# Performance work log

Hardware: AMD Instinct MI355X
Metric: run time of the kernel (lower is better)

## Reference

```python
import jax, jax.numpy as jnp
import numpy as np

NS, NC, T, NB = 32, 16, 64, 512
NSC = NS + NC


def setup_inputs() -> dict:
    key = jax.random.key(0)
    k1, k2, k3, k4, k5 = jax.random.split(key, 5)
    # SPD cost matrices so Quu is invertible (as assumed by the LQR math)
    L = jax.random.normal(k1, (NB, T, NSC, NSC), jnp.float32) * 0.1
    Q = L @ jnp.swapaxes(L, -1, -2) + jnp.eye(NSC, dtype=jnp.float32)
    p = jax.random.normal(k2, (NB, T, NSC), jnp.float32)
    x_init = jax.random.normal(k3, (NB, NS), jnp.float32)
    # stable-ish LTI dynamics
    A = 0.9 * jnp.eye(NS, dtype=jnp.float32) + 0.01 * jax.random.normal(k4, (NS, NS), jnp.float32)
    B = 0.1 * jax.random.normal(k5, (NS, NC), jnp.float32)
    dt = jnp.float32(0.1)
    return {"x_init": x_init, "Q": Q, "p": p, "A": A, "B": B, "dt": dt}


def _lqr(x_init, Q, p, A, B):
    ns, nc = A.shape[0], B.shape[1]
    nb, Th = Q.shape[0], Q.shape[1]
    dtype = Q.dtype

    # --- nominal rollout with zero control: x_{t+1} = A x_t ---
    def roll(x, _):
        return x @ A.T, x
    _, cx = jax.lax.scan(roll, x_init, None, length=Th)   # [T,B,ns] states x_0..x_{T-1}
    cu = jnp.zeros((Th, nb, nc), dtype)                    # current_u = 0
    xu = jnp.concatenate([cx, cu], -1)                     # [T,B,nsc]

    Qs = jnp.swapaxes(Q, 0, 1)                             # [T,B,nsc,nsc]
    ps = jnp.swapaxes(p, 0, 1)                             # [T,B,nsc]
    p_new = jnp.einsum('tbij,tbj->tbi', Qs, xu) + ps       # [T,B,nsc]

    F = jnp.concatenate([A, B], axis=1)                    # [ns, nsc]

    # --- backward Riccati recursion (V=v=0 at t=T-1 makes Qt=Q[T-1]) ---
    def bwd(carry, inp):
        V, v = carry                                       # [B,ns,ns], [B,ns]
        Qt_in, qt_in = inp
        Qt = Qt_in + jnp.einsum('si,bst,tj->bij', F, V, F)
        qt = qt_in + v @ F                                 # F^T v
        Qxx, Qxu = Qt[:, :ns, :ns], Qt[:, :ns, ns:]
        Qux, Quu = Qt[:, ns:, :ns], Qt[:, ns:, ns:]
        qx, qu = qt[:, :ns], qt[:, ns:]
        Quu_inv = jnp.linalg.pinv(Quu)
        Kt = -Quu_inv @ Qux                                # [B,nc,ns]
        kt = -jnp.einsum('bij,bj->bi', Quu_inv, qu)        # [B,nc]
        KtT = jnp.swapaxes(Kt, -1, -2)
        Vn = Qxx + Qxu @ Kt + KtT @ Qux + KtT @ Quu @ Kt
        vn = (qx + jnp.einsum('bij,bj->bi', Qxu, kt)
              + jnp.einsum('bij,bj->bi', KtT, qu)
              + jnp.einsum('bij,bj->bi', KtT @ Quu, kt))
        return (Vn, vn), (Kt, kt)

    V0 = jnp.zeros((nb, ns, ns), dtype)
    v0 = jnp.zeros((nb, ns), dtype)
    _, (Ks, ks) = jax.lax.scan(bwd, (V0, v0), (Qs, p_new), reverse=True)

    # --- forward rollout with feedback policy ---
    def fwd(carry, inp):
        xt, cost = carry
        Kt, kt, cxt, cut, Qt, pt = inp
        dut = jnp.einsum('bij,bj->bi', Kt, xt - cxt) + kt
        ut = dut + cut
        xut = jnp.concatenate([xt, ut], -1)
        cost = cost + 0.5 * jnp.einsum('bi,bij,bj->b', xut, Qt, xut) + (xut * pt).sum(-1)
        xn = xt @ A.T + ut @ B.T
        return (xn, cost), (xt, ut)

    (_, cost), (xs, us) = jax.lax.scan(
        fwd, (x_init, jnp.zeros(nb, dtype)), (Ks, ks, cx, cu, Qs, ps))
    x = jnp.swapaxes(xs, 0, 1)   # [B,T,ns]  (states x_0..x_{T-1}, matching x[...,:-1,:])
    u = jnp.swapaxes(us, 0, 1)   # [B,T,nc]
    return x, u, cost


def reference(x_init, Q, p, A, B, dt):
    # dt only matters for nonlinear relinearization; with constant LTI (A,B) it is unused.
    return _lqr(x_init, Q, p, A, B)
```

## Files before the change

kernel.cpp:

```cpp
#include <hip/hip_runtime.h>


#define NSd 32
#define NCd 16
#define Td 64
#define NBd 512
#define NSCd 48

typedef __bf16 bf16x8 __attribute__((ext_vector_type(8)));
typedef __bf16 bf16x4 __attribute__((ext_vector_type(4)));
typedef float f32x4 __attribute__((ext_vector_type(4)));

#define MFMA16(a, b, c) __builtin_amdgcn_mfma_f32_16x16x32_bf16(a, b, c, 0, 0, 0)

#define XOFF ((size_t)0)
#define UOFF ((size_t)NBd * Td * NSd)
#define COFF (UOFF + (size_t)NBd * Td * NCd)

__device__ __forceinline__ float rdl(float v, int l) {
  return __uint_as_float(__builtin_amdgcn_readlane(__float_as_uint(v), l));
}

__global__ __launch_bounds__(256, 3) void lqr_kernel(
    const float* __restrict__ x_init, const float* __restrict__ Qg,
    const float* __restrict__ pg, const float* __restrict__ Ag,
    const float* __restrict__ Bg, float* __restrict__ out,
    float* __restrict__ wsK, float* __restrict__ wskv) {
  const int b = blockIdx.x;
  const int tid = threadIdx.x;
  const int w = tid >> 6;
  const int lane = tid & 63;
  const int fn = lane & 15;
  const int quad = lane >> 4;
  const int k0 = quad * 8;

  __shared__ __attribute__((aligned(16))) float sQ[2304];
  __shared__ float scx[Td][NSd];
  __shared__ float sFf[NSd][NSCd];
  __shared__ __attribute__((aligned(16))) __bf16 sFTh[NSCd][32], sFTl[NSCd][32];
  __shared__ __attribute__((aligned(16))) __bf16 sVh[NSd][32], sVl[NSd][32];
  __shared__ __attribute__((aligned(16))) __bf16 sWTh[NSCd][32], sWTl[NSCd][32];
  __shared__ __attribute__((aligned(16))) __bf16 sXh[NSd][32], sXl[NSd][32];
  __shared__ __attribute__((aligned(16))) __bf16 sKTh[NSd][32], sKTl[NSd][32];
  __shared__ float sQuu[16][17];
  __shared__ float sqt[NSCd];
  __shared__ float svv[NSd];
  __shared__ __attribute__((aligned(16))) float sKT2[NSd][NCd];
  __shared__ float skt2[NCd], spf[2][NSCd];
  __shared__ float sxu[NSCd], sred[NSCd], ssx[NSd];

  for (int idx = tid; idx < 1536; idx += 256) {
    int i = idx / 48, j = idx - i * 48;
    sFf[i][j] = (j < 32) ? Ag[i * 32 + j] : Bg[i * 16 + (j - 32)];
  }
  for (int idx = tid; idx < 1536; idx += 256) {
    int a = idx >> 5, k = idx & 31;
    float f = (a < 32) ? Ag[k * 32 + a] : Bg[k * 16 + (a - 32)];
    __bf16 h = (__bf16)f;
    sFTh[a][k] = h;
    sFTl[a][k] = (__bf16)(f - (float)h);
  }
  for (int idx = tid; idx < 1024; idx += 256) {
    int r = idx >> 5, c = idx & 31;
    __bf16 z = (__bf16)0.f;
    sVh[r][c] = z; sVl[r][c] = z;
    sXh[r][c] = z; sXl[r][c] = z;
    sKTh[r][c] = z; sKTl[r][c] = z;
  }
  if (tid < 32) {
    float xi = x_init[b * 32 + tid];
    scx[0][tid] = xi;
    ssx[tid] = xi;
    svv[tid] = 0.f;
  }
  {
    const float4* src = (const float4*)(Qg + ((size_t)b * Td + 63) * 2304);
    float4* dst = (float4*)sQ;
    dst[tid] = src[tid];
    dst[tid + 256] = src[tid + 256];
    if (tid < 64) dst[tid + 512] = src[tid + 512];
  }
  float ppf = 0.f;
  if (w == 3 && lane < 48) ppf = pg[((size_t)b * Td + 63) * 48 + lane];
  __syncthreads();

  if (w == 0) {
    for (int t2 = 0; t2 < Td - 1; ++t2) {
      if (lane < 32) {
        float acc = 0.f;
#pragma unroll
        for (int j = 0; j < 32; j += 4) {
          float4 a4 = *(const float4*)&sFf[lane][j];
          acc += a4.x * scx[t2][j] + a4.y * scx[t2][j + 1] +
                 a4.z * scx[t2][j + 2] + a4.w * scx[t2][j + 3];
        }
        scx[t2 + 1][lane] = acc;
      }
    }
  }
  __syncthreads();

  for (int t = Td - 1; t >= 0; --t) {
    float4 pf0, pf1, pf2;
    float ppfn;
    if (t > 0) {
      const float4* src = (const float4*)(Qg + ((size_t)b * Td + (t - 1)) * 2304);
      pf0 = src[tid];
      pf1 = src[tid + 256];
      if (tid < 64) pf2 = src[tid + 512];
      if (w == 3 && lane < 48) ppfn = pg[((size_t)b * Td + t - 1) * 48 + lane];
    }
    if (w < 3) {
      const int I = w;
      bf16x8 aH = *(const bf16x8*)&sFTh[16 * I + fn][k0];
      bf16x8 aL = *(const bf16x8*)&sFTl[16 * I + fn][k0];
#pragma unroll
      for (int J = 0; J < 2; ++J) {
        bf16x8 bH = *(const bf16x8*)&sVh[16 * J + fn][k0];
        bf16x8 bL = *(const bf16x8*)&sVl[16 * J + fn][k0];
        f32x4 acc = {0.f, 0.f, 0.f, 0.f};
        acc = MFMA16(aL, bH, acc);
        acc = MFMA16(aH, bL, acc);
        acc = MFMA16(aH, bH, acc);
#pragma unroll
        for (int r = 0; r < 4; ++r) {
          float v = acc[r];
          __bf16 h = (__bf16)v;
          sWTh[16 * I + 4 * quad + r][16 * J + fn] = h;
          sWTl[16 * I + 4 * quad + r][16 * J + fn] = (__bf16)(v - (float)h);
        }
      }
    } else if (lane < 48) {
      float acc = ppf;
#pragma unroll
      for (int k = 0; k < 32; ++k) acc += sQ[k * 48 + lane] * scx[t][k];
#pragma unroll
      for (int k = 0; k < 32; ++k) acc += svv[k] * sFf[k][lane];
      sqt[lane] = acc;
    }
    if (t > 0 && w == 3) ppf = ppfn;
    __syncthreads();

    f32x4 accQ = {0.f, 0.f, 0.f, 0.f};
    if (w < 2) {
      const int I = w;
      bf16x8 aH = *(const bf16x8*)&sWTh[16 * I + fn][k0];
      bf16x8 aL = *(const bf16x8*)&sWTl[16 * I + fn][k0];
      {
        bf16x8 bH = *(const bf16x8*)&sFTh[16 * I + fn][k0];
        bf16x8 bL = *(const bf16x8*)&sFTl[16 * I + fn][k0];
#pragma unroll
        for (int r = 0; r < 4; ++r)
          accQ[r] = sQ[(16 * I + 4 * quad + r) * 48 + 16 * I + fn];
        accQ = MFMA16(aL, bH, accQ);
        accQ = MFMA16(aH, bL, accQ);
        accQ = MFMA16(aH, bH, accQ);
      }
      {
        bf16x8 bH = *(const bf16x8*)&sFTh[32 + fn][k0];
        bf16x8 bL = *(const bf16x8*)&sFTl[32 + fn][k0];
        f32x4 acc;
#pragma unroll
        for (int r = 0; r < 4; ++r)
          acc[r] = sQ[(16 * I + 4 * quad + r) * 48 + 32 + fn];
        acc = MFMA16(aL, bH, acc);
        acc = MFMA16(aH, bL, acc);
        acc = MFMA16(aH, bH, acc);
#pragma unroll
        for (int r = 0; r < 4; ++r) {
          float v = acc[r];
          __bf16 h = (__bf16)v;
          sXh[16 * I + 4 * quad + r][fn] = h;
          sXl[16 * I + 4 * quad + r][fn] = (__bf16)(v - (float)h);
        }
      }
    } else if (w == 2) {
      bf16x8 aH = *(const bf16x8*)&sWTh[fn][k0];
      bf16x8 aL = *(const bf16x8*)&sWTl[fn][k0];
      bf16x8 bH = *(const bf16x8*)&sFTh[16 + fn][k0];
      bf16x8 bL = *(const bf16x8*)&sFTl[16 + fn][k0];
#pragma unroll
      for (int r = 0; r < 4; ++r)
        accQ[r] = sQ[(4 * quad + r) * 48 + 16 + fn];
      accQ = MFMA16(aL, bH, accQ);
      accQ = MFMA16(aH, bL, accQ);
      accQ = MFMA16(aH, bH, accQ);
    } else {
      bf16x8 aH = *(const bf16x8*)&sWTh[32 + fn][k0];
      bf16x8 aL = *(const bf16x8*)&sWTl[32 + fn][k0];
      bf16x8 bH = *(const bf16x8*)&sFTh[32 + fn][k0];
      bf16x8 bL = *(const bf16x8*)&sFTl[32 + fn][k0];
      f32x4 acc;
#pragma unroll
      for (int r = 0; r < 4; ++r)
        acc[r] = sQ[(32 + 4 * quad + r) * 48 + 32 + fn];
      acc = MFMA16(aL, bH, acc);
      acc = MFMA16(aH, bL, acc);
      acc = MFMA16(aH, bH, acc);
#pragma unroll
      for (int r = 0; r < 4; ++r) sQuu[4 * quad + r][fn] = acc[r];
    }
    __syncthreads();

    if (t > 0) {
      float4* dst = (float4*)sQ;
      dst[tid] = pf0;
      dst[tid + 256] = pf1;
      if (tid < 64) dst[tid + 512] = pf2;
    }

    float rhs[16];
    if (lane < 32) {
      bf16x8 xh0 = *(const bf16x8*)&sXh[lane][0];
      bf16x8 xh1 = *(const bf16x8*)&sXh[lane][8];
      bf16x8 xl0 = *(const bf16x8*)&sXl[lane][0];
      bf16x8 xl1 = *(const bf16x8*)&sXl[lane][8];
#pragma unroll
      for (int i = 0; i < 8; ++i) {
        rhs[i] = (float)xh0[i] + (float)xl0[i];
        rhs[8 + i] = (float)xh1[i] + (float)xl1[i];
      }
    } else {
#pragma unroll
      for (int i = 0; i < 16; ++i) rhs[i] = sqt[32 + i];
    }
    float quu[16];
#pragma unroll
    for (int i = 0; i < 16; ++i) quu[i] = sQuu[i][fn];
#pragma unroll
    for (int r = 0; r < 15; ++r) {
      float inv = __builtin_amdgcn_rcpf(rdl(quu[r], r));
#pragma unroll
      for (int i = r + 1; i < 16; ++i) {
        float m = rdl(quu[i], r) * inv;
        rhs[i] -= m * rhs[r];
        quu[i] -= m * quu[r];
      }
    }
    float xx[16];
#pragma unroll
    for (int r = 15; r >= 0; --r) {
      float s = rhs[r];
#pragma unroll
      for (int c = r + 1; c < 16; ++c) s -= rdl(quu[r], c) * xx[c];
      xx[r] = s * __builtin_amdgcn_rcpf(rdl(quu[r], r));
    }
    if (lane < 32) {
      bf16x8 h0, l0, h1, l1;
#pragma unroll
      for (int u = 0; u < 8; ++u) {
        float kv = -xx[u];
        __bf16 hh = (__bf16)kv;
        h0[u] = hh; l0[u] = (__bf16)(kv - (float)hh);
        float kv2 = -xx[8 + u];
        __bf16 hh2 = (__bf16)kv2;
        h1[u] = hh2; l1[u] = (__bf16)(kv2 - (float)hh2);
      }
      *(bf16x8*)&sKTh[lane][0] = h0;
      *(bf16x8*)&sKTh[lane][8] = h1;
      *(bf16x8*)&sKTl[lane][0] = l0;
      *(bf16x8*)&sKTl[lane][8] = l1;
    }
    if (w == 0) {
      if (lane < 32) {
        float4* dst = (float4*)(wsK + (((size_t)b * Td + t) * 32 + lane) * 16);
        float4 v0 = {-xx[0], -xx[1], -xx[2], -xx[3]};
        float4 v1 = {-xx[4], -xx[5], -xx[6], -xx[7]};
        float4 v2 = {-xx[8], -xx[9], -xx[10], -xx[11]};
        float4 v3 = {-xx[12], -xx[13], -xx[14], -xx[15]};
        dst[0] = v0; dst[1] = v1; dst[2] = v2; dst[3] = v3;
      } else if (lane == 32) {
        float4* dst = (float4*)(wskv + ((size_t)b * Td + t) * 16);
        float4 v0 = {-xx[0], -xx[1], -xx[2], -xx[3]};
        float4 v1 = {-xx[4], -xx[5], -xx[6], -xx[7]};
        float4 v2 = {-xx[8], -xx[9], -xx[10], -xx[11]};
        float4 v3 = {-xx[12], -xx[13], -xx[14], -xx[15]};
        dst[0] = v0; dst[1] = v1; dst[2] = v2; dst[3] = v3;
      }
    }

    if (w == 0) {
      bf16x8 aH = *(const bf16x8*)&sXh[fn][k0];
      bf16x8 aL = *(const bf16x8*)&sXl[fn][k0];
      bf16x8 bH = *(const bf16x8*)&sKTh[fn][k0];
      bf16x8 bL = *(const bf16x8*)&sKTl[fn][k0];
      accQ = MFMA16(aL, bH, accQ);
      accQ = MFMA16(aH, bL, accQ);
      accQ = MFMA16(aH, bH, accQ);
#pragma unroll
      for (int r = 0; r < 4; ++r) {
        float v = accQ[r];
        __bf16 h = (__bf16)v;
        sVh[4 * quad + r][fn] = h;
        sVl[4 * quad + r][fn] = (__bf16)(v - (float)h);
      }
    } else if (w == 1) {
      bf16x8 aH = *(const bf16x8*)&sXh[16 + fn][k0];
      bf16x8 aL = *(const bf16x8*)&sXl[16 + fn][k0];
      bf16x8 bH = *(const bf16x8*)&sKTh[16 + fn][k0];
      bf16x8 bL = *(const bf16x8*)&sKTl[16 + fn][k0];
      accQ = MFMA16(aL, bH, accQ);
      accQ = MFMA16(aH, bL, accQ);
      accQ = MFMA16(aH, bH, accQ);
#pragma unroll
      for (int r = 0; r < 4; ++r) {
        float v = accQ[r];
        __bf16 h = (__bf16)v;
        sVh[16 + 4 * quad + r][16 + fn] = h;
        sVl[16 + 4 * quad + r][16 + fn] = (__bf16)(v - (float)h);
      }
    } else if (w == 2) {
      bf16x8 aH = *(const bf16x8*)&sXh[fn][k0];
      bf16x8 aL = *(const bf16x8*)&sXl[fn][k0];
      bf16x8 bH = *(const bf16x8*)&sKTh[16 + fn][k0];
      bf16x8 bL = *(const bf16x8*)&sKTl[16 + fn][k0];
      accQ = MFMA16(aL, bH, accQ);
      accQ = MFMA16(aH, bL, accQ);
      accQ = MFMA16(aH, bH, accQ);
      bf16x4 th, tl;
#pragma unroll
      for (int r = 0; r < 4; ++r) {
        float v = accQ[r];
        __bf16 h = (__bf16)v;
        __bf16 l = (__bf16)(v - (float)h);
        sVh[4 * quad + r][16 + fn] = h;
        sVl[4 * quad + r][16 + fn] = l;
        th[r] = h; tl[r] = l;
      }
      *(bf16x4*)&sVh[16 + fn][4 * quad] = th;
      *(bf16x4*)&sVl[16 + fn][4 * quad] = tl;
    } else {
      float acc = 0.f;
      bf16x8 xh0, xh1, xl0, xl1;
      if (lane < 32) {
        xh0 = *(const bf16x8*)&sXh[lane][0];
        xh1 = *(const bf16x8*)&sXh[lane][8];
        xl0 = *(const bf16x8*)&sXl[lane][0];
        xl1 = *(const bf16x8*)&sXl[lane][8];
        acc = sqt[lane];
      }
#pragma unroll
      for (int u = 0; u < 8; ++u) {
        float kt0 = -rdl(xx[u], 32);
        float kt1 = -rdl(xx[8 + u], 32);
        if (lane < 32) {
          acc += ((float)xh0[u] + (float)xl0[u]) * kt0;
          acc += ((float)xh1[u] + (float)xl1[u]) * kt1;
        }
      }
      if (lane < 32) svv[lane] = acc;
    }
    __syncthreads();
  }

  {
    const size_t kb = ((size_t)b * Td) << 9;
    if (tid < 128) {
      float4 v = ((const float4*)(wsK + kb))[tid];
      *(float4*)&sKT2[tid >> 2][(tid & 3) * 4] = v;
    } else if (tid < 144) {
      skt2[tid - 128] = wskv[((size_t)b * Td) * 16 + (tid - 128)];
    } else if (tid < 192) {
      spf[0][tid - 144] = pg[((size_t)b * Td) * 48 + (tid - 144)];
    }
  }
  __syncthreads();

  float costAcc = 0.f;
  float4 qpf0, qpf1, qpf2, kpf;
  float kkpf, ppf2;
  for (int t = 0; t < Td; ++t) {
    const int cur = t & 1, nxt = cur ^ 1;
    if (t > 0) {
      float4* dst = (float4*)sQ;
      dst[tid] = qpf0;
      dst[tid + 256] = qpf1;
      if (tid < 64) dst[tid + 512] = qpf2;
    }
    if (t < Td - 1) {
      const float4* src = (const float4*)(Qg + ((size_t)b * Td + t + 1) * 2304);
      qpf0 = src[tid];
      qpf1 = src[tid + 256];
      if (tid < 64) qpf2 = src[tid + 512];
      if (tid >= 128) {
        kpf = ((const float4*)(wsK + (((size_t)b * Td + t + 1) << 9)))[tid - 128];
      } else if (w == 1 && lane >= 32 && lane < 48) {
        kkpf = wskv[((size_t)b * Td + t + 1) * 16 + (lane - 32)];
        ppf2 = pg[((size_t)b * Td + t + 1) * 48 + 32 + (lane - 32)];
      } else if (w == 0 && lane >= 48) {
        ppf2 = pg[((size_t)b * Td + t + 1) * 48 + (lane - 48)];
      } else if (w == 1 && lane >= 48) {
        ppf2 = pg[((size_t)b * Td + t + 1) * 48 + 16 + (lane - 48)];
      }
    }
    if (w == 3) {
      if (lane < 16) {
        float acc = skt2[lane];
#pragma unroll
        for (int j = 0; j < 32; ++j)
          acc += sKT2[j][lane] * (ssx[j] - scx[t][j]);
        sxu[32 + lane] = acc;
        out[UOFF + ((size_t)b * Td + t) * 16 + lane] = acc;
      }
    } else if (w == 0) {
      if (lane < 32) {
        float xv = ssx[lane];
        sxu[lane] = xv;
        out[XOFF + ((size_t)b * Td + t) * 32 + lane] = xv;
      }
    } else if (w == 2) {
      float rv = (t > 0 && lane < 48) ? sred[lane] : 0.f;
      rv += __shfl_down(rv, 32);
      rv += __shfl_down(rv, 16);
      rv += __shfl_down(rv, 8);
      rv += __shfl_down(rv, 4);
      rv += __shfl_down(rv, 2);
      rv += __shfl_down(rv, 1);
      if (lane == 0) costAcc += rv;
    }
    __syncthreads();
    if (w == 0 && lane < 48) {
      float y = 0.f;
#pragma unroll
      for (int j = 0; j < 48; ++j) y += sQ[j * 48 + lane] * sxu[j];
      sred[lane] = sxu[lane] * (0.5f * y + spf[cur][lane]);
    } else if (w == 1 && lane < 32) {
      float acc = 0.f;
#pragma unroll
      for (int j = 0; j < 48; ++j) acc += sFf[lane][j] * sxu[j];
      ssx[lane] = acc;
    }
    if (t < Td - 1) {
      if (tid >= 128) {
        int i2 = tid - 128;
        *(float4*)&sKT2[i2 >> 2][(i2 & 3) * 4] = kpf;
      } else if (w == 1 && lane >= 32 && lane < 48) {
        skt2[lane - 32] = kkpf;
        spf[nxt][32 + (lane - 32)] = ppf2;
      } else if (w == 0 && lane >= 48) {
        spf[nxt][lane - 48] = ppf2;
      } else if (w == 1 && lane >= 48) {
        spf[nxt][16 + (lane - 48)] = ppf2;
      }
    }
    __syncthreads();
  }
  if (w == 2) {
    float rv = (lane < 48) ? sred[lane] : 0.f;
    rv += __shfl_down(rv, 32);
    rv += __shfl_down(rv, 16);
    rv += __shfl_down(rv, 8);
    rv += __shfl_down(rv, 4);
    rv += __shfl_down(rv, 2);
    rv += __shfl_down(rv, 1);
    if (lane == 0) out[COFF + b] = costAcc + rv;
  }
}

extern "C" void kernel_launch(void* const* d_in, const int* in_sizes, int n_in,
                              void* d_out, int out_size, void* d_ws, size_t ws_size,
                              hipStream_t stream) {
  const float* x_init = (const float*)d_in[0];
  const float* Qg = (const float*)d_in[1];
  const float* pg = (const float*)d_in[2];
  const float* Ag = (const float*)d_in[3];
  const float* Bg = (const float*)d_in[4];
  float* out = (float*)d_out;
  float* wsK = (float*)d_ws;
  float* wskv = wsK + (size_t)NBd * Td * NSd * NCd;
  lqr_kernel<<<NBd, 256, 0, stream>>>(x_init, Qg, pg, Ag, Bg, out, wsK, wskv);
}
```

Before: 762.2 us.

## Compute LQR cost analytically in backward pass and run forward rollout on one wave

Replaces the forward-pass cost accumulation, which reloaded every Q[t] from global memory, with an algebraic cost computed during the backward sweep from nominal-state terms and the -0.5 q_u^T Quu^-1 q_u term per step. The forward rollout now runs on a single wavefront with no block barriers and double-buffers K/k from the workspace. The Quu solve alternates between waves 2 and 3 with an extra barrier. Shared memory is merged into a union, and launch bounds are lowered to 2 blocks per SM. The analytic cost identity relies on the rollout matching the nominal trajectory (zero nominal control, exact LQR optimality), and the added barrier per step lengthens the backward pass.

```diff
diff --git a/kernel.cpp b/kernel.cpp
--- a/kernel.cpp
+++ b/kernel.cpp
@@ -21,7 +21,28 @@
   return __uint_as_float(__builtin_amdgcn_readlane(__float_as_uint(v), l));
 }
 
-__global__ __launch_bounds__(256, 3) void lqr_kernel(
+union LdsU {
+  struct {
+    __bf16 FTh[48][32], FTl[48][32];
+    __bf16 Vh[32][32], Vl[32][32];
+    __bf16 WTh[48][32], WTl[48][32];
+    __bf16 Xh[32][32], Xl[32][32];
+    __bf16 KTh[32][32], KTl[32][32];
+    float Quu[16][17];
+    float qt[48];
+    float vv[32];
+    float kt[16];
+  } bw;
+  struct {
+    float K2T[2][16 * 36];
+    float kv2[2][16];
+    float d[32];
+    float xs[32];
+    float uu[16];
+  } fw;
+};
+
+__global__ __launch_bounds__(256, 2) void lqr_kernel(
     const float* __restrict__ x_init, const float* __restrict__ Qg,
     const float* __restrict__ pg, const float* __restrict__ Ag,
     const float* __restrict__ Bg, float* __restrict__ out,
@@ -37,17 +58,8 @@
   __shared__ __attribute__((aligned(16))) float sQ[2304];
   __shared__ float scx[Td][NSd];
   __shared__ float sFf[NSd][NSCd];
-  __shared__ __attribute__((aligned(16))) __bf16 sFTh[NSCd][32], sFTl[NSCd][32];
-  __shared__ __attribute__((aligned(16))) __bf16 sVh[NSd][32], sVl[NSd][32];
-  __shared__ __attribute__((aligned(16))) __bf16 sWTh[NSCd][32], sWTl[NSCd][32];
-  __shared__ __attribute__((aligned(16))) __bf16 sXh[NSd][32], sXl[NSd][32];
-  __shared__ __attribute__((aligned(16))) __bf16 sKTh[NSd][32], sKTl[NSd][32];
-  __shared__ float sQuu[16][17];
-  __shared__ float sqt[NSCd];
-  __shared__ float svv[NSd];
-  __shared__ __attribute__((aligned(16))) float sKT2[NSd][NCd];
-  __shared__ float skt2[NCd], spf[2][NSCd];
-  __shared__ float sxu[NSCd], sred[NSCd], ssx[NSd];
+  __shared__ __attribute__((aligned(16))) LdsU U;
+  __shared__ float scostp[4];
 
   for (int idx = tid; idx < 1536; idx += 256) {
     int i = idx / 48, j = idx - i * 48;
@@ -57,21 +69,19 @@
     int a = idx >> 5, k = idx & 31;
     float f = (a < 32) ? Ag[k * 32 + a] : Bg[k * 16 + (a - 32)];
     __bf16 h = (__bf16)f;
-    sFTh[a][k] = h;
-    sFTl[a][k] = (__bf16)(f - (float)h);
+    U.bw.FTh[a][k] = h;
+    U.bw.FTl[a][k] = (__bf16)(f - (float)h);
   }
   for (int idx = tid; idx < 1024; idx += 256) {
     int r = idx >> 5, c = idx & 31;
     __bf16 z = (__bf16)0.f;
-    sVh[r][c] = z; sVl[r][c] = z;
-    sXh[r][c] = z; sXl[r][c] = z;
-    sKTh[r][c] = z; sKTl[r][c] = z;
+    U.bw.Vh[r][c] = z; U.bw.Vl[r][c] = z;
+    U.bw.Xh[r][c] = z; U.bw.Xl[r][c] = z;
+    U.bw.KTh[r][c] = z; U.bw.KTl[r][c] = z;
   }
   if (tid < 32) {
-    float xi = x_init[b * 32 + tid];
-    scx[0][tid] = xi;
-    ssx[tid] = xi;
-    svv[tid] = 0.f;
+    scx[0][tid] = x_init[b * 32 + tid];
+    U.bw.vv[tid] = 0.f;
   }
   {
     const float4* src = (const float4*)(Qg + ((size_t)b * Td + 63) * 2304);
@@ -100,7 +110,11 @@
   }
   __syncthreads();
 
+  float cAcc = 0.f;
+  float dAcc = 0.f;
+
   for (int t = Td - 1; t >= 0; --t) {
+    const int sw = 3 - (t & 1);
     float4 pf0, pf1, pf2;
     float ppfn;
     if (t > 0) {
@@ -112,12 +126,12 @@
     }
     if (w < 3) {
       const int I = w;
-      bf16x8 aH = *(const bf16x8*)&sFTh[16 * I + fn][k0];
-      bf16x8 aL = *(const bf16x8*)&sFTl[16 * I + fn][k0];
+      bf16x8 aH = *(const bf16x8*)&U.bw.FTh[16 * I + fn][k0];
+      bf16x8 aL = *(const bf16x8*)&U.bw.FTl[16 * I + fn][k0];
 #pragma unroll
       for (int J = 0; J < 2; ++J) {
-        bf16x8 bH = *(const bf16x8*)&sVh[16 * J + fn][k0];
-        bf16x8 bL = *(const bf16x8*)&sVl[16 * J + fn][k0];
+        bf16x8 bH = *(const bf16x8*)&U.bw.Vh[16 * J + fn][k0];
+        bf16x8 bL = *(const bf16x8*)&U.bw.Vl[16 * J + fn][k0];
         f32x4 acc = {0.f, 0.f, 0.f, 0.f};
         acc = MFMA16(aL, bH, acc);
         acc = MFMA16(aH, bL, acc);
@@ -126,17 +140,19 @@
         for (int r = 0; r < 4; ++r) {
           float v = acc[r];
           __bf16 h = (__bf16)v;
-          sWTh[16 * I + 4 * quad + r][16 * J + fn] = h;
-          sWTl[16 * I + 4 * quad + r][16 * J + fn] = (__bf16)(v - (float)h);
+          U.bw.WTh[16 * I + 4 * quad + r][16 * J + fn] = h;
+          U.bw.WTl[16 * I + 4 * quad + r][16 * J + fn] = (__bf16)(v - (float)h);
         }
       }
     } else if (lane < 48) {
-      float acc = ppf;
-#pragma unroll
-      for (int k = 0; k < 32; ++k) acc += sQ[k * 48 + lane] * scx[t][k];
-#pragma unroll
-      for (int k = 0; k < 32; ++k) acc += svv[k] * sFf[k][lane];
-      sqt[lane] = acc;
+      float acc1 = ppf;
+#pragma unroll
+      for (int k = 0; k < 32; ++k) acc1 += sQ[k * 48 + lane] * scx[t][k];
+      if (lane < 32) cAcc += 0.5f * scx[t][lane] * (acc1 + ppf);
+      float acc = acc1;
+#pragma unroll
+      for (int k = 0; k < 32; ++k) acc += U.bw.vv[k] * sFf[k][lane];
+      U.bw.qt[lane] = acc;
     }
     if (t > 0 && w == 3) ppf = ppfn;
     __syncthreads();
@@ -144,11 +160,11 @@
     f32x4 accQ = {0.f, 0.f, 0.f, 0.f};
     if (w < 2) {
       const int I = w;
-      bf16x8 aH = *(const bf16x8*)&sWTh[16 * I + fn][k0];
-      bf16x8 aL = *(const bf16x8*)&sWTl[16 * I + fn][k0];
+      bf16x8 aH = *(const bf16x8*)&U.bw.WTh[16 * I + fn][k0];
+      bf16x8 aL = *(const bf16x8*)&U.bw.WTl[16 * I + fn][k0];
       {
-        bf16x8 bH = *(const bf16x8*)&sFTh[16 * I + fn][k0];
-        bf16x8 bL = *(const bf16x8*)&sFTl[16 * I + fn][k0];
+        bf16x8 bH = *(const bf16x8*)&U.bw.FTh[16 * I + fn][k0];
+        bf16x8 bL = *(const bf16x8*)&U.bw.FTl[16 * I + fn][k0];
 #pragma unroll
         for (int r = 0; r < 4; ++r)
           accQ[r] = sQ[(16 * I + 4 * quad + r) * 48 + 16 * I + fn];
@@ -157,8 +173,8 @@
         accQ = MFMA16(aH, bH, accQ);
       }
       {
-        bf16x8 bH = *(const bf16x8*)&sFTh[32 + fn][k0];
-        bf16x8 bL = *(const bf16x8*)&sFTl[32 + fn][k0];
+        bf16x8 bH = *(const bf16x8*)&U.bw.FTh[32 + fn][k0];
+        bf16x8 bL = *(const bf16x8*)&U.bw.FTl[32 + fn][k0];
         f32x4 acc;
 #pragma unroll
         for (int r = 0; r < 4; ++r)
@@ -170,15 +186,15 @@
         for (int r = 0; r < 4; ++r) {
           float v = acc[r];
           __bf16 h = (__bf16)v;
-          sXh[16 * I + 4 * quad + r][fn] = h;
-          sXl[16 * I + 4 * quad + r][fn] = (__bf16)(v - (float)h);
+          U.bw.Xh[16 * I + 4 * quad + r][fn] = h;
+          U.bw.Xl[16 * I + 4 * quad + r][fn] = (__bf16)(v - (float)h);
         }
       }
     } else if (w == 2) {
-      bf16x8 aH = *(const bf16x8*)&sWTh[fn][k0];
-      bf16x8 aL = *(const bf16x8*)&sWTl[fn][k0];
-      bf16x8 bH = *(const bf16x8*)&sFTh[16 + fn][k0];
-      bf16x8 bL = *(const bf16x8*)&sFTl[16 + fn][k0];
+      bf16x8 aH = *(const bf16x8*)&U.bw.WTh[fn][k0];
+      bf16x8 aL = *(const bf16x8*)&U.bw.WTl[fn][k0];
+      bf16x8 bH = *(const bf16x8*)&U.bw.FTh[16 + fn][k0];
+      bf16x8 bL = *(const bf16x8*)&U.bw.FTl[16 + fn][k0];
 #pragma unroll
       for (int r = 0; r < 4; ++r)
         accQ[r] = sQ[(4 * quad + r) * 48 + 16 + fn];
@@ -186,10 +202,10 @@
       accQ = MFMA16(aH, bL, accQ);
       accQ = MFMA16(aH, bH, accQ);
     } else {
-      bf16x8 aH = *(const bf16x8*)&sWTh[32 + fn][k0];
-      bf16x8 aL = *(const bf16x8*)&sWTl[32 + fn][k0];
-      bf16x8 bH = *(const bf16x8*)&sFTh[32 + fn][k0];
-      bf16x8 bL = *(const bf16x8*)&sFTl[32 + fn][k0];
+      bf16x8 aH = *(const bf16x8*)&U.bw.WTh[32 + fn][k0];
+      bf16x8 aL = *(const bf16x8*)&U.bw.WTl[32 + fn][k0];
+      bf16x8 bH = *(const bf16x8*)&U.bw.FTh[32 + fn][k0];
+      bf16x8 bL = *(const bf16x8*)&U.bw.FTl[32 + fn][k0];
       f32x4 acc;
 #pragma unroll
       for (int r = 0; r < 4; ++r)
@@ -198,7 +214,7 @@
       acc = MFMA16(aH, bL, acc);
       acc = MFMA16(aH, bH, acc);
 #pragma unroll
-      for (int r = 0; r < 4; ++r) sQuu[4 * quad + r][fn] = acc[r];
+      for (int r = 0; r < 4; ++r) U.bw.Quu[4 * quad + r][fn] = acc[r];
     }
     __syncthreads();
 
@@ -209,60 +225,58 @@
       if (tid < 64) dst[tid + 512] = pf2;
     }
 
-    float rhs[16];
-    if (lane < 32) {
-      bf16x8 xh0 = *(const bf16x8*)&sXh[lane][0];
-      bf16x8 xh1 = *(const bf16x8*)&sXh[lane][8];
-      bf16x8 xl0 = *(const bf16x8*)&sXl[lane][0];
-      bf16x8 xl1 = *(const bf16x8*)&sXl[lane][8];
-#pragma unroll
-      for (int i = 0; i < 8; ++i) {
-        rhs[i] = (float)xh0[i] + (float)xl0[i];
-        rhs[8 + i] = (float)xh1[i] + (float)xl1[i];
-      }
-    } else {
-#pragma unroll
-      for (int i = 0; i < 16; ++i) rhs[i] = sqt[32 + i];
-    }
-    float quu[16];
-#pragma unroll
-    for (int i = 0; i < 16; ++i) quu[i] = sQuu[i][fn];
-#pragma unroll
-    for (int r = 0; r < 15; ++r) {
-      float inv = __builtin_amdgcn_rcpf(rdl(quu[r], r));
-#pragma unroll
-      for (int i = r + 1; i < 16; ++i) {
-        float m = rdl(quu[i], r) * inv;
-        rhs[i] -= m * rhs[r];
-        quu[i] -= m * quu[r];
-      }
-    }
-    float xx[16];
-#pragma unroll
-    for (int r = 15; r >= 0; --r) {
-      float s = rhs[r];
-#pragma unroll
-      for (int c = r + 1; c < 16; ++c) s -= rdl(quu[r], c) * xx[c];
-      xx[r] = s * __builtin_amdgcn_rcpf(rdl(quu[r], r));
-    }
-    if (lane < 32) {
-      bf16x8 h0, l0, h1, l1;
-#pragma unroll
-      for (int u = 0; u < 8; ++u) {
-        float kv = -xx[u];
-        __bf16 hh = (__bf16)kv;
-        h0[u] = hh; l0[u] = (__bf16)(kv - (float)hh);
-        float kv2 = -xx[8 + u];
-        __bf16 hh2 = (__bf16)kv2;
-        h1[u] = hh2; l1[u] = (__bf16)(kv2 - (float)hh2);
-      }
-      *(bf16x8*)&sKTh[lane][0] = h0;
-      *(bf16x8*)&sKTh[lane][8] = h1;
-      *(bf16x8*)&sKTl[lane][0] = l0;
-      *(bf16x8*)&sKTl[lane][8] = l1;
-    }
-    if (w == 0) {
-      if (lane < 32) {
+    if (w == sw) {
+      float rhs[16];
+      if (lane < 32) {
+        bf16x8 xh0 = *(const bf16x8*)&U.bw.Xh[lane][0];
+        bf16x8 xh1 = *(const bf16x8*)&U.bw.Xh[lane][8];
+        bf16x8 xl0 = *(const bf16x8*)&U.bw.Xl[lane][0];
+        bf16x8 xl1 = *(const bf16x8*)&U.bw.Xl[lane][8];
+#pragma unroll
+        for (int i = 0; i < 8; ++i) {
+          rhs[i] = (float)xh0[i] + (float)xl0[i];
+          rhs[8 + i] = (float)xh1[i] + (float)xl1[i];
+        }
+      } else {
+#pragma unroll
+        for (int i = 0; i < 16; ++i) rhs[i] = U.bw.qt[32 + i];
+      }
+      float quu[16];
+#pragma unroll
+      for (int i = 0; i < 16; ++i) quu[i] = U.bw.Quu[i][fn];
+#pragma unroll
+      for (int r = 0; r < 15; ++r) {
+        float inv = __builtin_amdgcn_rcpf(rdl(quu[r], r));
+#pragma unroll
+        for (int i = r + 1; i < 16; ++i) {
+          float m = rdl(quu[i], r) * inv;
+          rhs[i] -= m * rhs[r];
+          quu[i] -= m * quu[r];
+        }
+      }
+      float xx[16];
+#pragma unroll
+      for (int r = 15; r >= 0; --r) {
+        float s = rhs[r];
+#pragma unroll
+        for (int c = r + 1; c < 16; ++c) s -= rdl(quu[r], c) * xx[c];
+        xx[r] = s * __builtin_amdgcn_rcpf(rdl(quu[r], r));
+      }
+      if (lane < 32) {
+        bf16x8 h0, l0, h1, l1;
+#pragma unroll
+        for (int u = 0; u < 8; ++u) {
+          float kv = -xx[u];
+          __bf16 hh = (__bf16)kv;
+          h0[u] = hh; l0[u] = (__bf16)(kv - (float)hh);
+          float kv2 = -xx[8 + u];
+          __bf16 hh2 = (__bf16)kv2;
+          h1[u] = hh2; l1[u] = (__bf16)(kv2 - (float)hh2);
+        }
+        *(bf16x8*)&U.bw.KTh[lane][0] = h0;
+        *(bf16x8*)&U.bw.KTh[lane][8] = h1;
+        *(bf16x8*)&U.bw.KTl[lane][0] = l0;
+        *(bf16x8*)&U.bw.KTl[lane][8] = l1;
         float4* dst = (float4*)(wsK + (((size_t)b * Td + t) * 32 + lane) * 16);
         float4 v0 = {-xx[0], -xx[1], -xx[2], -xx[3]};
         float4 v1 = {-xx[4], -xx[5], -xx[6], -xx[7]};
@@ -270,20 +284,48 @@
         float4 v3 = {-xx[12], -xx[13], -xx[14], -xx[15]};
         dst[0] = v0; dst[1] = v1; dst[2] = v2; dst[3] = v3;
       } else if (lane == 32) {
+#pragma unroll
+        for (int u = 0; u < 16; ++u) U.bw.kt[u] = -xx[u];
         float4* dst = (float4*)(wskv + ((size_t)b * Td + t) * 16);
         float4 v0 = {-xx[0], -xx[1], -xx[2], -xx[3]};
         float4 v1 = {-xx[4], -xx[5], -xx[6], -xx[7]};
         float4 v2 = {-xx[8], -xx[9], -xx[10], -xx[11]};
         float4 v3 = {-xx[12], -xx[13], -xx[14], -xx[15]};
         dst[0] = v0; dst[1] = v1; dst[2] = v2; dst[3] = v3;
-      }
-    }
+        float s = 0.f;
+#pragma unroll
+        for (int i = 0; i < 16; ++i) s += U.bw.qt[32 + i] * xx[i];
+        dAcc -= 0.5f * s;
+      }
+      if (sw == 3) {
+        float acc = 0.f;
+        bf16x8 xh0, xh1, xl0, xl1;
+        if (lane < 32) {
+          xh0 = *(const bf16x8*)&U.bw.Xh[lane][0];
+          xh1 = *(const bf16x8*)&U.bw.Xh[lane][8];
+          xl0 = *(const bf16x8*)&U.bw.Xl[lane][0];
+          xl1 = *(const bf16x8*)&U.bw.Xl[lane][8];
+          acc = U.bw.qt[lane];
+        }
+#pragma unroll
+        for (int u = 0; u < 8; ++u) {
+          float kt0 = -rdl(xx[u], 32);
+          float kt1 = -rdl(xx[8 + u], 32);
+          if (lane < 32) {
+            acc += ((float)xh0[u] + (float)xl0[u]) * kt0;
+            acc += ((float)xh1[u] + (float)xl1[u]) * kt1;
+          }
+        }
+        if (lane < 32) U.bw.vv[lane] = acc;
+      }
+    }
+    __syncthreads();
 
     if (w == 0) {
-      bf16x8 aH = *(const bf16x8*)&sXh[fn][k0];
-      bf16x8 aL = *(const bf16x8*)&sXl[fn][k0];
-      bf16x8 bH = *(const bf16x8*)&sKTh[fn][k0];
-      bf16x8 bL = *(const bf16x8*)&sKTl[fn][k0];
+      bf16x8 aH = *(const bf16x8*)&U.bw.Xh[fn][k0];
+      bf16x8 aL = *(const bf16x8*)&U.bw.Xl[fn][k0];
+      bf16x8 bH = *(const bf16x8*)&U.bw.KTh[fn][k0];
+      bf16x8 bL = *(const bf16x8*)&U.bw.KTl[fn][k0];
       accQ = MFMA16(aL, bH, accQ);
       accQ = MFMA16(aH, bL, accQ);
       accQ = MFMA16(aH, bH, accQ);
@@ -291,14 +333,14 @@
       for (int r = 0; r < 4; ++r) {
         float v = accQ[r];
         __bf16 h = (__bf16)v;
-        sVh[4 * quad + r][fn] = h;
-        sVl[4 * quad + r][fn] = (__bf16)(v - (float)h);
+        U.bw.Vh[4 * quad + r][fn] = h;
+        U.bw.Vl[4 * quad + r][fn] = (__bf16)(v - (float)h);
       }
     } else if (w == 1) {
-      bf16x8 aH = *(const bf16x8*)&sXh[16 + fn][k0];
-      bf16x8 aL = *(const bf16x8*)&sXl[16 + fn][k0];
-      bf16x8 bH = *(const bf16x8*)&sKTh[16 + fn][k0];
-      bf16x8 bL = *(const bf16x8*)&sKTl[16 + fn][k0];
+      bf16x8 aH = *(const bf16x8*)&U.bw.Xh[16 + fn][k0];
+      bf16x8 aL = *(const bf16x8*)&U.bw.Xl[16 + fn][k0];
+      bf16x8 bH = *(const bf16x8*)&U.bw.KTh[16 + fn][k0];
+      bf16x8 bL = *(const bf16x8*)&U.bw.KTl[16 + fn][k0];
       accQ = MFMA16(aL, bH, accQ);
       accQ = MFMA16(aH, bL, accQ);
       accQ = MFMA16(aH, bH, accQ);
@@ -306,14 +348,14 @@
       for (int r = 0; r < 4; ++r) {
         float v = accQ[r];
         __bf16 h = (__bf16)v;
-        sVh[16 + 4 * quad + r][16 + fn] = h;
-        sVl[16 + 4 * quad + r][16 + fn] = (__bf16)(v - (float)h);
+        U.bw.Vh[16 + 4 * quad + r][16 + fn] = h;
+        U.bw.Vl[16 + 4 * quad + r][16 + fn] = (__bf16)(v - (float)h);
       }
     } else if (w == 2) {
-      bf16x8 aH = *(const bf16x8*)&sXh[fn][k0];
-      bf16x8 aL = *(const bf16x8*)&sXl[fn][k0];
-      bf16x8 bH = *(const bf16x8*)&sKTh[16 + fn][k0];
-      bf16x8 bL = *(const bf16x8*)&sKTl[16 + fn][k0];
+      bf16x8 aH = *(const bf16x8*)&U.bw.Xh[fn][k0];
+      bf16x8 aL = *(const bf16x8*)&U.bw.Xl[fn][k0];
+      bf16x8 bH = *(const bf16x8*)&U.bw.KTh[16 + fn][k0];
+      bf16x8 bL = *(const bf16x8*)&U.bw.KTl[16 + fn][k0];
       accQ = MFMA16(aL, bH, accQ);
       accQ = MFMA16(aH, bL, accQ);
       accQ = MFMA16(aH, bH, accQ);
@@ -323,137 +365,110 @@
         float v = accQ[r];
         __bf16 h = (__bf16)v;
         __bf16 l = (__bf16)(v - (float)h);
-        sVh[4 * quad + r][16 + fn] = h;
-        sVl[4 * quad + r][16 + fn] = l;
+        U.bw.Vh[4 * quad + r][16 + fn] = h;
+        U.bw.Vl[4 * quad + r][16 + fn] = l;
         th[r] = h; tl[r] = l;
       }
-      *(bf16x4*)&sVh[16 + fn][4 * quad] = th;
-      *(bf16x4*)&sVl[16 + fn][4 * quad] = tl;
-    } else {
-      float acc = 0.f;
-      bf16x8 xh0, xh1, xl0, xl1;
-      if (lane < 32) {
-        xh0 = *(const bf16x8*)&sXh[lane][0];
-        xh1 = *(const bf16x8*)&sXh[lane][8];
-        xl0 = *(const bf16x8*)&sXl[lane][0];
-        xl1 = *(const bf16x8*)&sXl[lane][8];
-        acc = sqt[lane];
-      }
-#pragma unroll
-      for (int u = 0; u < 8; ++u) {
-        float kt0 = -rdl(xx[u], 32);
-        float kt1 = -rdl(xx[8 + u], 32);
-        if (lane < 32) {
-          acc += ((float)xh0[u] + (float)xl0[u]) * kt0;
-          acc += ((float)xh1[u] + (float)xl1[u]) * kt1;
-        }
-      }
-      if (lane < 32) svv[lane] = acc;
+      *(bf16x4*)&U.bw.Vh[16 + fn][4 * quad] = th;
+      *(bf16x4*)&U.bw.Vl[16 + fn][4 * quad] = tl;
+    } else if (sw == 2) {
+      if (lane < 32) {
+        bf16x8 xh0 = *(const bf16x8*)&U.bw.Xh[lane][0];
+        bf16x8 xh1 = *(const bf16x8*)&U.bw.Xh[lane][8];
+        bf16x8 xl0 = *(const bf16x8*)&U.bw.Xl[lane][0];
+        bf16x8 xl1 = *(const bf16x8*)&U.bw.Xl[lane][8];
+        float acc = U.bw.qt[lane];
+#pragma unroll
+        for (int u = 0; u < 8; ++u) {
+          acc += ((float)xh0[u] + (float)xl0[u]) * U.bw.kt[u];
+          acc += ((float)xh1[u] + (float)xl1[u]) * U.bw.kt[8 + u];
+        }
+        U.bw.vv[lane] = acc;
+      }
     }
     __syncthreads();
   }
 
-  {
-    const size_t kb = ((size_t)b * Td) << 9;
-    if (tid < 128) {
-      float4 v = ((const float4*)(wsK + kb))[tid];
-      *(float4*)&sKT2[tid >> 2][(tid & 3) * 4] = v;
-    } else if (tid < 144) {
-      skt2[tid - 128] = wskv[((size_t)b * Td) * 16 + (tid - 128)];
-    } else if (tid < 192) {
-      spf[0][tid - 144] = pg[((size_t)b * Td) * 48 + (tid - 144)];
-    }
-  }
-  __syncthreads();
-
-  float costAcc = 0.f;
-  float4 qpf0, qpf1, qpf2, kpf;
-  float kkpf, ppf2;
-  for (int t = 0; t < Td; ++t) {
-    const int cur = t & 1, nxt = cur ^ 1;
-    if (t > 0) {
-      float4* dst = (float4*)sQ;
-      dst[tid] = qpf0;
-      dst[tid + 256] = qpf1;
-      if (tid < 64) dst[tid + 512] = qpf2;
-    }
-    if (t < Td - 1) {
-      const float4* src = (const float4*)(Qg + ((size_t)b * Td + t + 1) * 2304);
-      qpf0 = src[tid];
-      qpf1 = src[tid + 256];
-      if (tid < 64) qpf2 = src[tid + 512];
-      if (tid >= 128) {
-        kpf = ((const float4*)(wsK + (((size_t)b * Td + t + 1) << 9)))[tid - 128];
-      } else if (w == 1 && lane >= 32 && lane < 48) {
-        kkpf = wskv[((size_t)b * Td + t + 1) * 16 + (lane - 32)];
-        ppf2 = pg[((size_t)b * Td + t + 1) * 48 + 32 + (lane - 32)];
-      } else if (w == 0 && lane >= 48) {
-        ppf2 = pg[((size_t)b * Td + t + 1) * 48 + (lane - 48)];
-      } else if (w == 1 && lane >= 48) {
-        ppf2 = pg[((size_t)b * Td + t + 1) * 48 + 16 + (lane - 48)];
-      }
-    }
-    if (w == 3) {
-      if (lane < 16) {
-        float acc = skt2[lane];
-#pragma unroll
-        for (int j = 0; j < 32; ++j)
-          acc += sKT2[j][lane] * (ssx[j] - scx[t][j]);
-        sxu[32 + lane] = acc;
-        out[UOFF + ((size_t)b * Td + t) * 16 + lane] = acc;
-      }
-    } else if (w == 0) {
-      if (lane < 32) {
-        float xv = ssx[lane];
-        sxu[lane] = xv;
-        out[XOFF + ((size_t)b * Td + t) * 32 + lane] = xv;
-      }
-    } else if (w == 2) {
-      float rv = (t > 0 && lane < 48) ? sred[lane] : 0.f;
-      rv += __shfl_down(rv, 32);
-      rv += __shfl_down(rv, 16);
-      rv += __shfl_down(rv, 8);
-      rv += __shfl_down(rv, 4);
-      rv += __shfl_down(rv, 2);
-      rv += __shfl_down(rv, 1);
-      if (lane == 0) costAcc += rv;
-    }
-    __syncthreads();
-    if (w == 0 && lane < 48) {
-      float y = 0.f;
-#pragma unroll
-      for (int j = 0; j < 48; ++j) y += sQ[j * 48 + lane] * sxu[j];
-      sred[lane] = sxu[lane] * (0.5f * y + spf[cur][lane]);
-    } else if (w == 1 && lane < 32) {
-      float acc = 0.f;
-#pragma unroll
-      for (int j = 0; j < 48; ++j) acc += sFf[lane][j] * sxu[j];
-      ssx[lane] = acc;
-    }
-    if (t < Td - 1) {
-      if (tid >= 128) {
-        int i2 = tid - 128;
-        *(float4*)&sKT2[i2 >> 2][(i2 & 3) * 4] = kpf;
-      } else if (w == 1 && lane >= 32 && lane < 48) {
-        skt2[lane - 32] = kkpf;
-        spf[nxt][32 + (lane - 32)] = ppf2;
-      } else if (w == 0 && lane >= 48) {
-        spf[nxt][lane - 48] = ppf2;
-      } else if (w == 1 && lane >= 48) {
-        spf[nxt][16 + (lane - 48)] = ppf2;
-      }
-    }
-    __syncthreads();
-  }
-  if (w == 2) {
-    float rv = (lane < 48) ? sred[lane] : 0.f;
+  if (w == 3) {
+    float rv = (lane < 32) ? cAcc : 0.f;
     rv += __shfl_down(rv, 32);
     rv += __shfl_down(rv, 16);
     rv += __shfl_down(rv, 8);
     rv += __shfl_down(rv, 4);
     rv += __shfl_down(rv, 2);
     rv += __shfl_down(rv, 1);
-    if (lane == 0) out[COFF + b] = costAcc + rv;
+    if (lane == 0) scostp[0] = rv;
+  }
+  if (lane == 32 && w >= 2) scostp[w - 1] = dAcc;
+  __syncthreads();
+
+  if (w == 0) {
+    {
+      const float4* src = (const float4*)(wsK + ((size_t)b * Td) * 512);
+      float4 ka = src[lane * 2], kb = src[lane * 2 + 1];
+      int jj = lane >> 1, ib = (lane & 1) * 8;
+      float* kt2 = U.fw.K2T[0];
+      kt2[(ib + 0) * 36 + jj] = ka.x; kt2[(ib + 1) * 36 + jj] = ka.y;
+      kt2[(ib + 2) * 36 + jj] = ka.z; kt2[(ib + 3) * 36 + jj] = ka.w;
+      kt2[(ib + 4) * 36 + jj] = kb.x; kt2[(ib + 5) * 36 + jj] = kb.y;
+      kt2[(ib + 6) * 36 + jj] = kb.z; kt2[(ib + 7) * 36 + jj] = kb.w;
+      if (lane < 16) U.fw.kv2[0][lane] = wskv[(size_t)b * Td * 16 + lane];
+    }
+    float xr = (lane < 32) ? scx[0][lane] : 0.f;
+    for (int t = 0; t < Td; ++t) {
+      const int cur = t & 1, nxt = cur ^ 1;
+      float4 pa, pb;
+      float pk;
+      if (t < Td - 1) {
+        const float4* src = (const float4*)(wsK + ((size_t)b * Td + t + 1) * 512);
+        pa = src[lane * 2];
+        pb = src[lane * 2 + 1];
+        if (lane < 16) pk = wskv[((size_t)b * Td + t + 1) * 16 + lane];
+      }
+      if (lane < 32) {
+        U.fw.d[lane] = xr - scx[t][lane];
+        U.fw.xs[lane] = xr;
+        out[XOFF + ((size_t)b * Td + t) * 32 + lane] = xr;
+      }
+      if (lane < 16) {
+        float uv = U.fw.kv2[cur][lane];
+        const float* kr = &U.fw.K2T[cur][lane * 36];
+#pragma unroll
+        for (int j4 = 0; j4 < 8; ++j4) {
+          float4 kk = *(const float4*)&kr[j4 * 4];
+          float4 dd = *(const float4*)&U.fw.d[j4 * 4];
+          uv += kk.x * dd.x + kk.y * dd.y + kk.z * dd.z + kk.w * dd.w;
+        }
+        U.fw.uu[lane] = uv;
+        out[UOFF + ((size_t)b * Td + t) * 16 + lane] = uv;
+      }
+      if (lane < 32) {
+        float acc = 0.f;
+#pragma unroll
+        for (int j4 = 0; j4 < 8; ++j4) {
+          float4 ff = *(const float4*)&sFf[lane][j4 * 4];
+          float4 xv = *(const float4*)&U.fw.xs[j4 * 4];
+          acc += ff.x * xv.x + ff.y * xv.y + ff.z * xv.z + ff.w * xv.w;
+        }
+#pragma unroll
+        for (int j4 = 0; j4 < 4; ++j4) {
+          float4 ff = *(const float4*)&sFf[lane][32 + j4 * 4];
+          float4 uv = *(const float4*)&U.fw.uu[j4 * 4];
+          acc += ff.x * uv.x + ff.y * uv.y + ff.z * uv.z + ff.w * uv.w;
+        }
+        xr = acc;
+      }
+      if (t < Td - 1) {
+        int jj = lane >> 1, ib = (lane & 1) * 8;
+        float* kt2 = U.fw.K2T[nxt];
+        kt2[(ib + 0) * 36 + jj] = pa.x; kt2[(ib + 1) * 36 + jj] = pa.y;
+        kt2[(ib + 2) * 36 + jj] = pa.z; kt2[(ib + 3) * 36 + jj] = pa.w;
+        kt2[(ib + 4) * 36 + jj] = pb.x; kt2[(ib + 5) * 36 + jj] = pb.y;
+        kt2[(ib + 6) * 36 + jj] = pb.z; kt2[(ib + 7) * 36 + jj] = pb.w;
+        if (lane < 16) U.fw.kv2[nxt][lane] = pk;
+      }
+    }
+    if (lane == 0) out[COFF + b] = scostp[0] + scostp[1] + scostp[2];
   }
 }
 
```

Measured after the change: 667.7 us. 12.4% less time.
